# Kernel tuning notes

Hardware: AMD Instinct MI355X
Metric: run time of the kernel (lower is better)

Reference implementation:

```python
import jax, jax.numpy as jnp
import numpy as np

N = 100000
E = 1600000
CIN = 32
COUT = 32
K = 5
EPS = 1e-15      # PyG GMMConv EPS in sigma^2 denominator
BN_EPS = 1e-5    # torch BatchNorm1d default eps


def gmm_conv(x, edge_index, edge_attr, g, mu, sigma, root, bias):
    """PyG GMMConv (MoNet), aggr='mean', root_weight=True, bias=True."""
    src, dst = edge_index[0], edge_index[1]
    n = x.shape[0]
    k = mu.shape[0]
    cout = root.shape[1]
    xg = (x @ g).reshape(n, k, cout)                # [N, K, out]
    xj = xg[src]                                    # gather: [E, K, out]
    d = edge_attr[:, None, :] - mu[None, :, :]      # [E, K, 3]
    w = jnp.exp(-0.5 * jnp.sum(d * d / (EPS + sigma[None] ** 2), axis=-1))  # [E, K]
    msg = jnp.einsum('eko,ek->eo', xj, w)           # [E, out]
    agg = jax.ops.segment_sum(msg, dst, num_segments=n)
    cnt = jax.ops.segment_sum(jnp.ones((msg.shape[0],), x.dtype), dst, num_segments=n)
    agg = agg / jnp.clip(cnt, 1.0)[:, None]         # mean aggregation
    return agg + x @ root + bias


def batch_norm(x, gamma, beta):
    # training-mode BatchNorm1d: biased batch statistics over node dim
    m = x.mean(0)
    v = x.var(0)
    return (x - m) * jax.lax.rsqrt(v + BN_EPS) * gamma + beta


def setup_inputs() -> dict:
    key = jax.random.key(0)
    ks = jax.random.split(key, 12)
    p = lambda k, s, sc=0.1: jax.random.normal(k, s, jnp.float32) * sc
    return {
        'x': jax.random.normal(ks[0], (N, CIN), jnp.float32),
        'edge_index': jax.random.randint(ks[1], (2, E), 0, N, jnp.int32),
        'edge_attr': jax.random.uniform(ks[2], (E, 3), jnp.float32),
        # left conv1: in -> out, K=5
        'g1': p(ks[3], (CIN, K * COUT)), 'mu1': p(ks[4], (K, 3), 1.0), 'sigma1': jnp.ones((K, 3), jnp.float32),
        'root1': p(ks[5], (CIN, COUT)), 'b1': jnp.zeros((COUT,), jnp.float32),
        'gam1': jnp.ones((COUT,), jnp.float32), 'bet1': jnp.zeros((COUT,), jnp.float32),
        # left conv2: out -> out, K=5
        'g2': p(ks[6], (COUT, K * COUT)), 'mu2': p(ks[7], (K, 3), 1.0), 'sigma2': jnp.ones((K, 3), jnp.float32),
        'root2': p(ks[8], (COUT, COUT)), 'b2': jnp.zeros((COUT,), jnp.float32),
        'gam2': jnp.ones((COUT,), jnp.float32), 'bet2': jnp.zeros((COUT,), jnp.float32),
        # shortcut conv: in -> out, K=1
        'gs': p(ks[9], (CIN, 1 * COUT)), 'mus': p(ks[10], (1, 3), 1.0), 'sigmas': jnp.ones((1, 3), jnp.float32),
        'roots': p(ks[11], (CIN, COUT)), 'bs': jnp.zeros((COUT,), jnp.float32),
        'gams': jnp.ones((COUT,), jnp.float32), 'bets': jnp.zeros((COUT,), jnp.float32),
    }


def reference(x, edge_index, edge_attr,
              g1, mu1, sigma1, root1, b1, gam1, bet1,
              g2, mu2, sigma2, root2, b2, gam2, bet2,
              gs, mus, sigmas, roots, bs, gams, bets):
    h = jax.nn.elu(batch_norm(gmm_conv(x, edge_index, edge_attr, g1, mu1, sigma1, root1, b1), gam1, bet1))
    h = batch_norm(gmm_conv(h, edge_index, edge_attr, g2, mu2, sigma2, root2, b2), gam2, bet2)
    s = batch_norm(gmm_conv(x, edge_index, edge_attr, gs, mus, sigmas, roots, bs), gams, bets)
    return jax.nn.elu(h + s)
```

## Files before the change

kernel.cpp:

```cpp
#include <hip/hip_runtime.h>
#include <hip/hip_bf16.h>
#include <math.h>


#define ELU(v) ((v) > 0.f ? (v) : (__expf(v) - 1.f))

using short8  = __attribute__((ext_vector_type(8))) short;
using floatx4 = __attribute__((ext_vector_type(4))) float;

__device__ inline ushort f2bf(float f) {
    __hip_bfloat16 h = __float2bfloat16(f);
    return *reinterpret_cast<ushort*>(&h);
}
__device__ inline float bflo(unsigned u) { return __uint_as_float(u << 16); }
__device__ inline float bfhi(unsigned u) { return __uint_as_float(u & 0xffff0000u); }
__device__ inline unsigned pack_bf2(float lo, float hi) {
    return ((unsigned)f2bf(hi) << 16) | (unsigned)f2bf(lo);
}

__global__ __launch_bounds__(256) void prep_a(
    const float* __restrict__ x, unsigned* __restrict__ AGGb, int N)
{
    const int idx = blockIdx.x * blockDim.x + threadIdx.x;
    if (idx >= N * 16) return;
    const int n = idx >> 4, l = idx & 15;
    const float2 p = ((const float2*)x)[idx];
    AGGb[(size_t)n * 112 + 96 + l] = pack_bf2(p.x, p.y);
}

__global__ __launch_bounds__(256) void prep_b(
    const float* __restrict__ out1, const float* __restrict__ coef,
    unsigned* __restrict__ AGGb, int N)
{
    const int idx = blockIdx.x * blockDim.x + threadIdx.x;
    if (idx >= N * 16) return;
    const int n = idx >> 4, l = idx & 15;
    const float2 p = ((const float2*)out1)[idx];
    const int c0 = 2 * l, c1 = 2 * l + 1;
    float v0 = p.x * coef[c0] + coef[32 + c0];
    float v1 = p.y * coef[c1] + coef[32 + c1];
    v0 = ELU(v0); v1 = ELU(v1);
    AGGb[(size_t)n * 96 + 80 + l] = pack_bf2(v0, v1);
}

#define CH 4096
__global__ __launch_bounds__(256) void binfill_k(
    const int* __restrict__ ei, const float* __restrict__ attr,
    int* __restrict__ gcur, unsigned long long* __restrict__ pay0,
    int E, int NB, int CAPc)
{
    __shared__ unsigned long long srec[CH];
    __shared__ unsigned char sbin[CH];
    __shared__ int cnt[256], offs[256], wcur[256], gbase[256], sc[256];

    const int t = threadIdx.x;
    const int e0 = blockIdx.x * CH;
    const int nrec = min(CH, E - e0);

    cnt[t] = 0;
    __syncthreads();

    unsigned long long rec[16];
    int bin[16];
#pragma unroll
    for (int r = 0; r < 16; ++r) {
        const int e = e0 + r * 256 + t;
        bin[r] = -1;
        if (e < E) {
            const int s = ei[e], d = ei[E + e];
            const float a0 = attr[(size_t)e * 3 + 0];
            const float a1 = attr[(size_t)e * 3 + 1];
            const float a2 = attr[(size_t)e * 3 + 2];
            const unsigned q0 = (unsigned)min(max((int)(a0 * 4096.f), 0), 4095);
            const unsigned q1 = (unsigned)min(max((int)(a1 * 4096.f), 0), 4095);
            const unsigned q2 = (unsigned)min(max((int)(a2 * 4096.f), 0), 4095);
            rec[r] = (unsigned long long)(unsigned)s
                   | ((unsigned long long)(d & 511) << 17)
                   | ((unsigned long long)q0 << 26)
                   | ((unsigned long long)q1 << 38)
                   | ((unsigned long long)q2 << 50);
            bin[r] = d >> 9;
            atomicAdd(&cnt[bin[r]], 1);
        }
    }
    __syncthreads();

    const int v = cnt[t];
    sc[t] = v;
    __syncthreads();
    for (int o = 1; o < 256; o <<= 1) {
        const int xx = (t >= o) ? sc[t - o] : 0;
        __syncthreads();
        sc[t] += xx;
        __syncthreads();
    }
    offs[t] = sc[t] - v;
    wcur[t] = sc[t] - v;
    __syncthreads();

#pragma unroll
    for (int r = 0; r < 16; ++r) {
        if (bin[r] >= 0) {
            const int pos = atomicAdd(&wcur[bin[r]], 1);
            srec[pos] = rec[r];
            sbin[pos] = (unsigned char)bin[r];
        }
    }
    __syncthreads();

    if (t < NB && cnt[t] > 0) gbase[t] = atomicAdd(&gcur[t], cnt[t]);
    __syncthreads();

    for (int i = t; i < nrec; i += 256) {
        const int b = sbin[i];
        const int idx = gbase[b] + (i - offs[b]);
        if (idx < CAPc)
            pay0[(size_t)b * CAPc + idx] = srec[i];
    }
}

__global__ void bucket_scan(const int* __restrict__ gcur, int* __restrict__ bbase,
                            int NB)
{
    __shared__ int sh[256];
    const int t = threadIdx.x;
    const int v = (t < NB) ? gcur[t] : 0;
    sh[t] = v;
    __syncthreads();
    for (int o = 1; o < 256; o <<= 1) {
        const int xx = (t >= o) ? sh[t - o] : 0;
        __syncthreads();
        sh[t] += xx;
        __syncthreads();
    }
    if (t < NB) bbase[t] = sh[t] - v;
}

__global__ __launch_bounds__(256) void scatter2_k(
    const unsigned long long* __restrict__ pay0, const int* __restrict__ gcur,
    const int* __restrict__ bbase, int* __restrict__ row_ptr,
    unsigned long long* __restrict__ pay, int N, int CAPc, int NB)
{
    const int b = blockIdx.x;
    const int t = threadIdx.x;
    const int d0 = b << 9;
    const int nd = min(512, N - d0);

    __shared__ int cnt[512];
    __shared__ int offs[512];
    __shared__ int sscan[256];

    for (int i = t; i < 512; i += 256) cnt[i] = 0;
    __syncthreads();

    const int total = min(gcur[b], CAPc);
    const unsigned long long* src = pay0 + (size_t)b * CAPc;

    for (int i = t; i < total; i += 256) {
        const int dlo = (int)((src[i] >> 17) & 511);
        atomicAdd(&cnt[dlo], 1);
    }
    __syncthreads();

    const int c0 = cnt[2 * t], c1 = cnt[2 * t + 1];
    const int pairsum = c0 + c1;
    sscan[t] = pairsum;
    __syncthreads();
    for (int o = 1; o < 256; o <<= 1) {
        const int xx = (t >= o) ? sscan[t - o] : 0;
        __syncthreads();
        sscan[t] += xx;
        __syncthreads();
    }
    const int excl = sscan[t] - pairsum;
    offs[2 * t] = excl;
    offs[2 * t + 1] = excl + c0;
    __syncthreads();
    const int btotal = sscan[255];

    const int base = bbase[b];
    for (int i = t; i < nd; i += 256) row_ptr[d0 + i] = base + offs[i];
    if (b == NB - 1 && t == 0) row_ptr[N] = base + btotal;

    for (int i = t; i < 512; i += 256) cnt[i] = offs[i];
    __syncthreads();

    for (int i = t; i < total; i += 256) {
        const unsigned long long rec = src[i];
        const int dlo = (int)((rec >> 17) & 511);
        const int p = atomicAdd(&cnt[dlo], 1);
        pay[base + p] = rec;
    }
}

template <int SLS, bool HAS_S>
__global__ __launch_bounds__(256) void gather_k(
    const unsigned* __restrict__ XB,
    const unsigned long long* __restrict__ payload,
    const int* __restrict__ row_ptr,
    const float* __restrict__ mu_m, const float* __restrict__ sg_m,
    const float* __restrict__ mu_s, const float* __restrict__ sg_s,
    unsigned* __restrict__ AGGb,
    int N, int ntiles)
{
    constexpr int KS = HAS_S ? 6 : 5;
    constexpr float DQ = 1.0f / 4096.0f;

    float mm[15], im[15];
#pragma unroll
    for (int i = 0; i < 15; ++i) {
        mm[i] = mu_m[i];
        float s = sg_m[i];
        im[i] = 1.0f / (1e-15f + s * s);
    }
    float ms[3], is[3];
    if (HAS_S) {
#pragma unroll
        for (int i = 0; i < 3; ++i) {
            ms[i] = mu_s[i];
            float s = sg_s[i];
            is[i] = 1.0f / (1e-15f + s * s);
        }
    }

    const int l = threadIdx.x & 15;
    const int g = threadIdx.x >> 4;
    __shared__ float wbuf[16][17][8];

    for (int tile = blockIdx.x; tile < ntiles; tile += gridDim.x) {
        const int dst = tile * 16 + g;
        float2 acc[KS];
#pragma unroll
        for (int k = 0; k < KS; ++k) acc[k] = make_float2(0.f, 0.f);

        int rp0 = 0, deg = 0;
        if (dst < N) { rp0 = row_ptr[dst]; deg = row_ptr[dst + 1] - rp0; }

        auto body = [&](int j) {
            const float4 a = *(const float4*)&wbuf[g][j][0];
            const float4 b = *(const float4*)&wbuf[g][j][4];
            const int sj = __float_as_int(a.x);
            const unsigned u = XB[(size_t)sj * 16 + l];
            const float x0 = bflo(u), x1 = bfhi(u);
            acc[0].x = fmaf(a.y, x0, acc[0].x); acc[0].y = fmaf(a.y, x1, acc[0].y);
            acc[1].x = fmaf(a.z, x0, acc[1].x); acc[1].y = fmaf(a.z, x1, acc[1].y);
            acc[2].x = fmaf(a.w, x0, acc[2].x); acc[2].y = fmaf(a.w, x1, acc[2].y);
            acc[3].x = fmaf(b.x, x0, acc[3].x); acc[3].y = fmaf(b.x, x1, acc[3].y);
            acc[4].x = fmaf(b.y, x0, acc[4].x); acc[4].y = fmaf(b.y, x1, acc[4].y);
            if (HAS_S) {
                acc[5].x = fmaf(b.z, x0, acc[5].x); acc[5].y = fmaf(b.z, x1, acc[5].y);
            }
        };

        for (int base = 0; base < deg; base += 16) {
            const int nj = min(16, deg - base);
            if (l < nj) {
                unsigned long long pq = payload[rp0 + base + l];
                const int src = (int)(pq & 0x1FFFFull);
                float p0 = ((int)((pq >> 26) & 0xFFF) + 0.5f) * DQ;
                float p1 = ((int)((pq >> 38) & 0xFFF) + 0.5f) * DQ;
                float p2 = ((int)((pq >> 50) & 0xFFF) + 0.5f) * DQ;
                float w[5], wS = 0.f;
#pragma unroll
                for (int k = 0; k < 5; ++k) {
                    float d0 = p0 - mm[k * 3 + 0];
                    float d1 = p1 - mm[k * 3 + 1];
                    float d2 = p2 - mm[k * 3 + 2];
                    float q = d0 * d0 * im[k * 3 + 0] + d1 * d1 * im[k * 3 + 1]
                            + d2 * d2 * im[k * 3 + 2];
                    w[k] = __expf(-0.5f * q);
                }
                if (HAS_S) {
                    float d0 = p0 - ms[0], d1 = p1 - ms[1], d2 = p2 - ms[2];
                    float q = d0 * d0 * is[0] + d1 * d1 * is[1] + d2 * d2 * is[2];
                    wS = __expf(-0.5f * q);
                }
                float4* wp = (float4*)&wbuf[g][l][0];
                wp[0] = make_float4(__int_as_float(src), w[0], w[1], w[2]);
                wp[1] = make_float4(w[3], w[4], wS, 0.f);
            }
            int j = 0;
            for (; j + 3 < nj; j += 4) { body(j); body(j + 1); body(j + 2); body(j + 3); }
            for (; j < nj; ++j) body(j);
        }

        if (dst < N) {
            const float invd = 1.0f / fmaxf((float)deg, 1.0f);
            unsigned* out = AGGb + (size_t)dst * (SLS * 16) + l;
#pragma unroll
            for (int k = 0; k < KS; ++k)
                out[k * 16] = pack_bf2(acc[k].x * invd, acc[k].y * invd);
        }
    }
}

template <bool HAS_S>
__global__ __launch_bounds__(256) void transform_k(
    const unsigned* __restrict__ AGGb,
    const float* __restrict__ g,
    const float* __restrict__ rootm,
    const float* __restrict__ bm,
    const float* __restrict__ gss,
    const float* __restrict__ rootss,
    const float* __restrict__ bss,
    float* __restrict__ out_m, float* __restrict__ out_s,
    float* __restrict__ stats_m, float* __restrict__ stats_s,
    int N)
{
    constexpr int SLS = HAS_S ? 7 : 6;
    const int lane = threadIdx.x & 63;
    const int l4 = lane & 15, quad = lane >> 4;
    const int wv = threadIdx.x >> 6;

    short8 Bc[6][2];
#pragma unroll
    for (int s = 0; s < 5; ++s)
#pragma unroll
        for (int t = 0; t < 2; ++t)
#pragma unroll
            for (int j = 0; j < 8; ++j)
                Bc[s][t][j] = (short)f2bf(g[(quad * 8 + j) * 160 + s * 32 + 16 * t + l4]);
#pragma unroll
    for (int t = 0; t < 2; ++t)
#pragma unroll
        for (int j = 0; j < 8; ++j)
            Bc[5][t][j] = (short)f2bf(rootm[(quad * 8 + j) * 32 + 16 * t + l4]);

    short8 Bs2[2][2];
    if (HAS_S) {
#pragma unroll
        for (int t = 0; t < 2; ++t)
#pragma unroll
            for (int j = 0; j < 8; ++j) {
                Bs2[0][t][j] = (short)f2bf(gss[(quad * 8 + j) * 32 + 16 * t + l4]);
                Bs2[1][t][j] = (short)f2bf(rootss[(quad * 8 + j) * 32 + 16 * t + l4]);
            }
    }

    const float bm0 = bm[l4], bm1 = bm[16 + l4];
    const float bs0 = HAS_S ? bss[l4] : 0.f;
    const float bs1 = HAS_S ? bss[16 + l4] : 0.f;

    const int ngroups = (N + 15) >> 4;
    float ps0 = 0, pq0 = 0, ps1 = 0, pq1 = 0;
    float psS0 = 0, pqS0 = 0, psS1 = 0, pqS1 = 0;

    for (int grp = blockIdx.x * 4 + wv; grp < ngroups; grp += gridDim.x * 4) {
        const int node0 = grp * 16;
        const int myn = min(node0 + l4, N - 1);
        const unsigned* arow = AGGb + (size_t)myn * (SLS * 16) + quad * 4;

        floatx4 acc0 = {0.f, 0.f, 0.f, 0.f}, acc1 = {0.f, 0.f, 0.f, 0.f};
#pragma unroll
        for (int s = 0; s < 6; ++s) {
            const int slot = (s < 5) ? s : (SLS - 1);
            const uint4 av = *(const uint4*)(arow + 16 * slot);
            const short8 A = *reinterpret_cast<const short8*>(&av);
            acc0 = __builtin_amdgcn_mfma_f32_16x16x32_bf16(A, Bc[s][0], acc0, 0, 0, 0);
            acc1 = __builtin_amdgcn_mfma_f32_16x16x32_bf16(A, Bc[s][1], acc1, 0, 0, 0);
        }
        floatx4 accS0 = {0.f, 0.f, 0.f, 0.f}, accS1 = {0.f, 0.f, 0.f, 0.f};
        if (HAS_S) {
#pragma unroll
            for (int s = 0; s < 2; ++s) {
                const int slot = 5 + s;
                const uint4 av = *(const uint4*)(arow + 16 * slot);
                const short8 A = *reinterpret_cast<const short8*>(&av);
                accS0 = __builtin_amdgcn_mfma_f32_16x16x32_bf16(A, Bs2[s][0], accS0, 0, 0, 0);
                accS1 = __builtin_amdgcn_mfma_f32_16x16x32_bf16(A, Bs2[s][1], accS1, 0, 0, 0);
            }
        }

#pragma unroll
        for (int r = 0; r < 4; ++r) {
            const int n = node0 + quad * 4 + r;
            if (n < N) {
                float v0 = acc0[r] + bm0;
                float v1 = acc1[r] + bm1;
                out_m[(size_t)n * 32 + l4] = v0;
                out_m[(size_t)n * 32 + 16 + l4] = v1;
                ps0 += v0; pq0 += v0 * v0;
                ps1 += v1; pq1 += v1 * v1;
                if (HAS_S) {
                    float s0 = accS0[r] + bs0;
                    float s1 = accS1[r] + bs1;
                    out_s[(size_t)n * 32 + l4] = s0;
                    out_s[(size_t)n * 32 + 16 + l4] = s1;
                    psS0 += s0; pqS0 += s0 * s0;
                    psS1 += s1; pqS1 += s1 * s1;
                }
            }
        }
    }

    __shared__ float sred[64];
    const int tid = threadIdx.x;
    const int spread = (blockIdx.x & 7) * 64;
    {
        if (tid < 64) sred[tid] = 0.f;
        __syncthreads();
        atomicAdd(&sred[l4], ps0);       atomicAdd(&sred[16 + l4], ps1);
        atomicAdd(&sred[32 + l4], pq0);  atomicAdd(&sred[48 + l4], pq1);
        __syncthreads();
        if (tid < 64) atomicAdd(&stats_m[spread + tid], sred[tid]);
        __syncthreads();
    }
    if (HAS_S) {
        if (tid < 64) sred[tid] = 0.f;
        __syncthreads();
        atomicAdd(&sred[l4], psS0);      atomicAdd(&sred[16 + l4], psS1);
        atomicAdd(&sred[32 + l4], pqS0); atomicAdd(&sred[48 + l4], pqS1);
        __syncthreads();
        if (tid < 64) atomicAdd(&stats_s[spread + tid], sred[tid]);
    }
}

__global__ void coef_k(const float* __restrict__ stats, const float* __restrict__ gam,
                       const float* __restrict__ bet, float* __restrict__ coef,
                       float invN)
{
    int c = threadIdx.x;
    if (c < 32) {
        float s = 0.f, q = 0.f;
        for (int p = 0; p < 8; ++p) { s += stats[p * 64 + c]; q += stats[p * 64 + 32 + c]; }
        float m = s * invN;
        float v = fmaxf(q * invN - m * m, 0.f);
        float sc = gam[c] * rsqrtf(v + 1e-5f);
        coef[c] = sc;
        coef[32 + c] = bet[c] - m * sc;
    }
}

__global__ __launch_bounds__(256) void final_k(
    const float* __restrict__ o2, const float* __restrict__ os,
    const float* __restrict__ c2, const float* __restrict__ cs,
    float* __restrict__ out, int total)
{
    int idx = blockIdx.x * blockDim.x + threadIdx.x;
    if (idx >= total) return;
    int c = idx & 31;
    float v = o2[idx] * c2[c] + c2[32 + c] + os[idx] * cs[c] + cs[32 + c];
    out[idx] = ELU(v);
}

extern "C" void kernel_launch(void* const* d_in, const int* in_sizes, int n_in,
                              void* d_out, int out_size, void* d_ws, size_t ws_size,
                              hipStream_t stream)
{
    const float* x      = (const float*)d_in[0];
    const int*   ei     = (const int*)d_in[1];
    const float* attr   = (const float*)d_in[2];
    const float* g1     = (const float*)d_in[3];
    const float* mu1    = (const float*)d_in[4];
    const float* sig1   = (const float*)d_in[5];
    const float* root1  = (const float*)d_in[6];
    const float* b1     = (const float*)d_in[7];
    const float* gam1   = (const float*)d_in[8];
    const float* bet1   = (const float*)d_in[9];
    const float* g2     = (const float*)d_in[10];
    const float* mu2    = (const float*)d_in[11];
    const float* sig2   = (const float*)d_in[12];
    const float* root2  = (const float*)d_in[13];
    const float* b2     = (const float*)d_in[14];
    const float* gam2   = (const float*)d_in[15];
    const float* bet2   = (const float*)d_in[16];
    const float* gs     = (const float*)d_in[17];
    const float* mus    = (const float*)d_in[18];
    const float* sigs   = (const float*)d_in[19];
    const float* roots  = (const float*)d_in[20];
    const float* bs     = (const float*)d_in[21];
    const float* gams   = (const float*)d_in[22];
    const float* bets   = (const float*)d_in[23];

    const int N = in_sizes[0] / 32;
    const int E = in_sizes[1] / 2;
    const int total = N * 32;
    const int ntiles = (N + 15) / 16;
    const int NB = (N + 511) >> 9;
    const int CAPc = ((((E + NB - 1) / NB) * 5) / 4 + 15) & ~15;

    char* ws = (char*)d_ws;
    size_t off = 0;
    auto carve = [&](size_t bytes) {
        void* p = ws + off;
        off = (off + bytes + 255) & ~(size_t)255;
        return p;
    };
    unsigned* XB   = (unsigned*)carve((size_t)N * 16 * 4);
    unsigned* AGGb = (unsigned*)carve((size_t)N * 112 * 4);
    float*  OUT1   = (float*)carve((size_t)N * 32 * 4);
    float*  OUT2   = (float*)carve((size_t)N * 32 * 4);
    float*  OUTS   = (float*)carve((size_t)N * 32 * 4);
    unsigned long long* PAY  = (unsigned long long*)carve((size_t)E * 8);
    unsigned long long* PAY0 = (unsigned long long*)carve((size_t)NB * CAPc * 8);
    int*    ROWP   = (int*)carve((size_t)(N + 1) * 4);
    int*    GCUR   = (int*)carve(512 * 4);
    int*    BBASE  = GCUR + 256;
    float*  STATS  = (float*)carve(3 * 512 * 4);
    float*  COEF   = (float*)carve(3 * 64 * 4);
    float* stats1 = STATS, *stats2 = STATS + 512, *statsS = STATS + 1024;
    float* coef1 = COEF, *coef2 = COEF + 64, *coefS = COEF + 128;
    (void)ws_size; (void)n_in; (void)out_size;

    const float invN = 1.0f / (float)N;
    const int ew = (total + 255) / 256;
    const int epb = (N * 16 + 255) / 256;
    const int nfb = (E + CH - 1) / CH;

    hipMemsetAsync(GCUR, 0, 256 * 4, stream);
    hipMemsetAsync(STATS, 0, 3 * 512 * 4, stream);

    binfill_k<<<nfb, 256, 0, stream>>>(ei, attr, GCUR, PAY0, E, NB, CAPc);
    bucket_scan<<<1, 256, 0, stream>>>(GCUR, BBASE, NB);
    scatter2_k<<<NB, 256, 0, stream>>>(PAY0, GCUR, BBASE, ROWP, PAY, N, CAPc, NB);

    prep_a<<<epb, 256, 0, stream>>>(x, AGGb, N);
    {
    }
    extern __global__ void prep_xb(const float*, unsigned*, int);
    prep_xb<<<epb, 256, 0, stream>>>(x, XB, N);

    gather_k<7, true><<<ntiles, 256, 0, stream>>>(XB, PAY, ROWP,
        mu1, sig1, mus, sigs, AGGb, N, ntiles);
    transform_k<true><<<1024, 256, 0, stream>>>(AGGb, g1, root1, b1,
        gs, roots, bs, OUT1, OUTS, stats1, statsS, N);
    coef_k<<<1, 64, 0, stream>>>(stats1, gam1, bet1, coef1, invN);
    coef_k<<<1, 64, 0, stream>>>(statsS, gams, bets, coefS, invN);

    prep_b<<<epb, 256, 0, stream>>>(OUT1, coef1, AGGb, N);
    extern __global__ void prep_hxb(const float*, const float*, unsigned*, int);
    prep_hxb<<<epb, 256, 0, stream>>>(OUT1, coef1, XB, N);
    gather_k<6, false><<<ntiles, 256, 0, stream>>>(XB, PAY, ROWP,
        mu2, sig2, nullptr, nullptr, AGGb, N, ntiles);
    transform_k<false><<<1024, 256, 0, stream>>>(AGGb, g2, root2, b2,
        nullptr, nullptr, nullptr, OUT2, nullptr, stats2, nullptr, N);
    coef_k<<<1, 64, 0, stream>>>(stats2, gam2, bet2, coef2, invN);

    final_k<<<ew, 256, 0, stream>>>(OUT2, OUTS, coef2, coefS, (float*)d_out, total);
}

__global__ __launch_bounds__(256) void prep_xb(
    const float* __restrict__ x, unsigned* __restrict__ XB, int N)
{
    const int idx = blockIdx.x * blockDim.x + threadIdx.x;
    if (idx >= N * 16) return;
    const float2 p = ((const float2*)x)[idx];
    XB[idx] = pack_bf2(p.x, p.y);
}

__global__ __launch_bounds__(256) void prep_hxb(
    const float* __restrict__ out1, const float* __restrict__ coef,
    unsigned* __restrict__ XB, int N)
{
    const int idx = blockIdx.x * blockDim.x + threadIdx.x;
    if (idx >= N * 16) return;
    const int l = idx & 15;
    const float2 p = ((const float2*)out1)[idx];
    const int c0 = 2 * l, c1 = 2 * l + 1;
    float v0 = p.x * coef[c0] + coef[32 + c0];
    float v1 = p.y * coef[c1] + coef[32 + c1];
    v0 = ELU(v0); v1 = ELU(v1);
    XB[idx] = pack_bf2(v0, v1);
}
```

Before: 326.5 us.

## Fuse edge gather and MFMA transform into one kernel via shared-memory staging

Merges the per-destination gather/aggregation kernel and the MFMA feature-transform kernel into a single kernel. Each block aggregates 16 nodes into a shared-memory tile and then applies the bf16 MFMA transform directly from LDS. This removes the AGGb global round-trip and the prep_a/prep_b copy kernels. The cost is extra LDS use, a block barrier between the two phases, and one tile per block instead of a persistent loop, so some waves sit idle during the MMA phase.

```diff
diff --git a/kernel.cpp b/kernel.cpp
--- a/kernel.cpp
+++ b/kernel.cpp
@@ -18,29 +18,28 @@
     return ((unsigned)f2bf(hi) << 16) | (unsigned)f2bf(lo);
 }
 
-__global__ __launch_bounds__(256) void prep_a(
-    const float* __restrict__ x, unsigned* __restrict__ AGGb, int N)
+__global__ __launch_bounds__(256) void prep_xb(
+    const float* __restrict__ x, unsigned* __restrict__ XB, int N)
 {
     const int idx = blockIdx.x * blockDim.x + threadIdx.x;
     if (idx >= N * 16) return;
-    const int n = idx >> 4, l = idx & 15;
     const float2 p = ((const float2*)x)[idx];
-    AGGb[(size_t)n * 112 + 96 + l] = pack_bf2(p.x, p.y);
-}
-
-__global__ __launch_bounds__(256) void prep_b(
+    XB[idx] = pack_bf2(p.x, p.y);
+}
+
+__global__ __launch_bounds__(256) void prep_hxb(
     const float* __restrict__ out1, const float* __restrict__ coef,
-    unsigned* __restrict__ AGGb, int N)
+    unsigned* __restrict__ XB, int N)
 {
     const int idx = blockIdx.x * blockDim.x + threadIdx.x;
     if (idx >= N * 16) return;
-    const int n = idx >> 4, l = idx & 15;
+    const int l = idx & 15;
     const float2 p = ((const float2*)out1)[idx];
     const int c0 = 2 * l, c1 = 2 * l + 1;
     float v0 = p.x * coef[c0] + coef[32 + c0];
     float v1 = p.y * coef[c1] + coef[32 + c1];
     v0 = ELU(v0); v1 = ELU(v1);
-    AGGb[(size_t)n * 96 + 80 + l] = pack_bf2(v0, v1);
+    XB[idx] = pack_bf2(v0, v1);
 }
 
 #define CH 4096
@@ -193,110 +192,13 @@
     }
 }
 
-template <int SLS, bool HAS_S>
-__global__ __launch_bounds__(256) void gather_k(
+template <bool HAS_S>
+__global__ __launch_bounds__(256) void gt_k(
     const unsigned* __restrict__ XB,
     const unsigned long long* __restrict__ payload,
     const int* __restrict__ row_ptr,
     const float* __restrict__ mu_m, const float* __restrict__ sg_m,
     const float* __restrict__ mu_s, const float* __restrict__ sg_s,
-    unsigned* __restrict__ AGGb,
-    int N, int ntiles)
-{
-    constexpr int KS = HAS_S ? 6 : 5;
-    constexpr float DQ = 1.0f / 4096.0f;
-
-    float mm[15], im[15];
-#pragma unroll
-    for (int i = 0; i < 15; ++i) {
-        mm[i] = mu_m[i];
-        float s = sg_m[i];
-        im[i] = 1.0f / (1e-15f + s * s);
-    }
-    float ms[3], is[3];
-    if (HAS_S) {
-#pragma unroll
-        for (int i = 0; i < 3; ++i) {
-            ms[i] = mu_s[i];
-            float s = sg_s[i];
-            is[i] = 1.0f / (1e-15f + s * s);
-        }
-    }
-
-    const int l = threadIdx.x & 15;
-    const int g = threadIdx.x >> 4;
-    __shared__ float wbuf[16][17][8];
-
-    for (int tile = blockIdx.x; tile < ntiles; tile += gridDim.x) {
-        const int dst = tile * 16 + g;
-        float2 acc[KS];
-#pragma unroll
-        for (int k = 0; k < KS; ++k) acc[k] = make_float2(0.f, 0.f);
-
-        int rp0 = 0, deg = 0;
-        if (dst < N) { rp0 = row_ptr[dst]; deg = row_ptr[dst + 1] - rp0; }
-
-        auto body = [&](int j) {
-            const float4 a = *(const float4*)&wbuf[g][j][0];
-            const float4 b = *(const float4*)&wbuf[g][j][4];
-            const int sj = __float_as_int(a.x);
-            const unsigned u = XB[(size_t)sj * 16 + l];
-            const float x0 = bflo(u), x1 = bfhi(u);
-            acc[0].x = fmaf(a.y, x0, acc[0].x); acc[0].y = fmaf(a.y, x1, acc[0].y);
-            acc[1].x = fmaf(a.z, x0, acc[1].x); acc[1].y = fmaf(a.z, x1, acc[1].y);
-            acc[2].x = fmaf(a.w, x0, acc[2].x); acc[2].y = fmaf(a.w, x1, acc[2].y);
-            acc[3].x = fmaf(b.x, x0, acc[3].x); acc[3].y = fmaf(b.x, x1, acc[3].y);
-            acc[4].x = fmaf(b.y, x0, acc[4].x); acc[4].y = fmaf(b.y, x1, acc[4].y);
-            if (HAS_S) {
-                acc[5].x = fmaf(b.z, x0, acc[5].x); acc[5].y = fmaf(b.z, x1, acc[5].y);
-            }
-        };
-
-        for (int base = 0; base < deg; base += 16) {
-            const int nj = min(16, deg - base);
-            if (l < nj) {
-                unsigned long long pq = payload[rp0 + base + l];
-                const int src = (int)(pq & 0x1FFFFull);
-                float p0 = ((int)((pq >> 26) & 0xFFF) + 0.5f) * DQ;
-                float p1 = ((int)((pq >> 38) & 0xFFF) + 0.5f) * DQ;
-                float p2 = ((int)((pq >> 50) & 0xFFF) + 0.5f) * DQ;
-                float w[5], wS = 0.f;
-#pragma unroll
-                for (int k = 0; k < 5; ++k) {
-                    float d0 = p0 - mm[k * 3 + 0];
-                    float d1 = p1 - mm[k * 3 + 1];
-                    float d2 = p2 - mm[k * 3 + 2];
-                    float q = d0 * d0 * im[k * 3 + 0] + d1 * d1 * im[k * 3 + 1]
-                            + d2 * d2 * im[k * 3 + 2];
-                    w[k] = __expf(-0.5f * q);
-                }
-                if (HAS_S) {
-                    float d0 = p0 - ms[0], d1 = p1 - ms[1], d2 = p2 - ms[2];
-                    float q = d0 * d0 * is[0] + d1 * d1 * is[1] + d2 * d2 * is[2];
-                    wS = __expf(-0.5f * q);
-                }
-                float4* wp = (float4*)&wbuf[g][l][0];
-                wp[0] = make_float4(__int_as_float(src), w[0], w[1], w[2]);
-                wp[1] = make_float4(w[3], w[4], wS, 0.f);
-            }
-            int j = 0;
-            for (; j + 3 < nj; j += 4) { body(j); body(j + 1); body(j + 2); body(j + 3); }
-            for (; j < nj; ++j) body(j);
-        }
-
-        if (dst < N) {
-            const float invd = 1.0f / fmaxf((float)deg, 1.0f);
-            unsigned* out = AGGb + (size_t)dst * (SLS * 16) + l;
-#pragma unroll
-            for (int k = 0; k < KS; ++k)
-                out[k * 16] = pack_bf2(acc[k].x * invd, acc[k].y * invd);
-        }
-    }
-}
-
-template <bool HAS_S>
-__global__ __launch_bounds__(256) void transform_k(
-    const unsigned* __restrict__ AGGb,
     const float* __restrict__ g,
     const float* __restrict__ rootm,
     const float* __restrict__ bm,
@@ -307,112 +209,170 @@
     float* __restrict__ stats_m, float* __restrict__ stats_s,
     int N)
 {
-    constexpr int SLS = HAS_S ? 7 : 6;
-    const int lane = threadIdx.x & 63;
-    const int l4 = lane & 15, quad = lane >> 4;
-    const int wv = threadIdx.x >> 6;
-
-    short8 Bc[6][2];
-#pragma unroll
-    for (int s = 0; s < 5; ++s)
-#pragma unroll
-        for (int t = 0; t < 2; ++t)
+    constexpr int KS = HAS_S ? 6 : 5;
+    constexpr int SLS = KS + 1;
+    constexpr int STRIDE = SLS * 16 + 4;
+    constexpr float DQ = 1.0f / 4096.0f;
+
+    __shared__ float wbuf[16][17][8];
+    __shared__ unsigned sA[16 * STRIDE];
+    __shared__ float sred[128];
+
+    const int tid = threadIdx.x;
+    const int l = tid & 15, grp = tid >> 4;
+    const int lane = tid & 63, l4 = lane & 15, quad = lane >> 4;
+    const int wv = tid >> 6;
+    const int half = wv & 1;
+
+    if (tid < 128) sred[tid] = 0.f;
+
+    const bool convRole = (wv < 2);
+    const bool sRole = HAS_S && (wv >= 2);
+    short8 Bf[6];
+    float bias0 = 0.f;
+    if (convRole) {
+#pragma unroll
+        for (int s = 0; s < 5; ++s)
 #pragma unroll
             for (int j = 0; j < 8; ++j)
-                Bc[s][t][j] = (short)f2bf(g[(quad * 8 + j) * 160 + s * 32 + 16 * t + l4]);
-#pragma unroll
-    for (int t = 0; t < 2; ++t)
+                Bf[s][j] = (short)f2bf(g[(quad * 8 + j) * 160 + s * 32 + 16 * half + l4]);
 #pragma unroll
         for (int j = 0; j < 8; ++j)
-            Bc[5][t][j] = (short)f2bf(rootm[(quad * 8 + j) * 32 + 16 * t + l4]);
-
-    short8 Bs2[2][2];
+            Bf[5][j] = (short)f2bf(rootm[(quad * 8 + j) * 32 + 16 * half + l4]);
+        bias0 = bm[16 * half + l4];
+    } else if (sRole) {
+#pragma unroll
+        for (int j = 0; j < 8; ++j) {
+            Bf[0][j] = (short)f2bf(gss[(quad * 8 + j) * 32 + 16 * half + l4]);
+            Bf[1][j] = (short)f2bf(rootss[(quad * 8 + j) * 32 + 16 * half + l4]);
+        }
+        bias0 = bss[16 * half + l4];
+    }
+
+    float mm[15], im[15];
+#pragma unroll
+    for (int i = 0; i < 15; ++i) {
+        mm[i] = mu_m[i];
+        float s = sg_m[i];
+        im[i] = 1.0f / (1e-15f + s * s);
+    }
+    float ms[3], is[3];
     if (HAS_S) {
 #pragma unroll
-        for (int t = 0; t < 2; ++t)
-#pragma unroll
-            for (int j = 0; j < 8; ++j) {
-                Bs2[0][t][j] = (short)f2bf(gss[(quad * 8 + j) * 32 + 16 * t + l4]);
-                Bs2[1][t][j] = (short)f2bf(rootss[(quad * 8 + j) * 32 + 16 * t + l4]);
+        for (int i = 0; i < 3; ++i) {
+            ms[i] = mu_s[i];
+            float s = sg_s[i];
+            is[i] = 1.0f / (1e-15f + s * s);
+        }
+    }
+
+    const int dst = blockIdx.x * 16 + grp;
+    float2 acc[KS];
+#pragma unroll
+    for (int k = 0; k < KS; ++k) acc[k] = make_float2(0.f, 0.f);
+
+    int rp0 = 0, deg = 0;
+    if (dst < N) { rp0 = row_ptr[dst]; deg = row_ptr[dst + 1] - rp0; }
+
+    auto body = [&](int j) {
+        const float4 a = *(const float4*)&wbuf[grp][j][0];
+        const float4 b = *(const float4*)&wbuf[grp][j][4];
+        const int sj = __float_as_int(a.x);
+        const unsigned u = XB[(size_t)sj * 16 + l];
+        const float x0 = bflo(u), x1 = bfhi(u);
+        acc[0].x = fmaf(a.y, x0, acc[0].x); acc[0].y = fmaf(a.y, x1, acc[0].y);
+        acc[1].x = fmaf(a.z, x0, acc[1].x); acc[1].y = fmaf(a.z, x1, acc[1].y);
+        acc[2].x = fmaf(a.w, x0, acc[2].x); acc[2].y = fmaf(a.w, x1, acc[2].y);
+        acc[3].x = fmaf(b.x, x0, acc[3].x); acc[3].y = fmaf(b.x, x1, acc[3].y);
+        acc[4].x = fmaf(b.y, x0, acc[4].x); acc[4].y = fmaf(b.y, x1, acc[4].y);
+        if (HAS_S) {
+            acc[5].x = fmaf(b.z, x0, acc[5].x); acc[5].y = fmaf(b.z, x1, acc[5].y);
+        }
+    };
+
+    for (int base = 0; base < deg; base += 16) {
+        const int nj = min(16, deg - base);
+        if (l < nj) {
+            unsigned long long pq = payload[rp0 + base + l];
+            const int src = (int)(pq & 0x1FFFFull);
+            float p0 = ((int)((pq >> 26) & 0xFFF) + 0.5f) * DQ;
+            float p1 = ((int)((pq >> 38) & 0xFFF) + 0.5f) * DQ;
+            float p2 = ((int)((pq >> 50) & 0xFFF) + 0.5f) * DQ;
+            float w[5], wS = 0.f;
+#pragma unroll
+            for (int k = 0; k < 5; ++k) {
+                float d0 = p0 - mm[k * 3 + 0];
+                float d1 = p1 - mm[k * 3 + 1];
+                float d2 = p2 - mm[k * 3 + 2];
+                float q = d0 * d0 * im[k * 3 + 0] + d1 * d1 * im[k * 3 + 1]
+                        + d2 * d2 * im[k * 3 + 2];
+                w[k] = __expf(-0.5f * q);
             }
-    }
-
-    const float bm0 = bm[l4], bm1 = bm[16 + l4];
-    const float bs0 = HAS_S ? bss[l4] : 0.f;
-    const float bs1 = HAS_S ? bss[16 + l4] : 0.f;
-
-    const int ngroups = (N + 15) >> 4;
-    float ps0 = 0, pq0 = 0, ps1 = 0, pq1 = 0;
-    float psS0 = 0, pqS0 = 0, psS1 = 0, pqS1 = 0;
-
-    for (int grp = blockIdx.x * 4 + wv; grp < ngroups; grp += gridDim.x * 4) {
-        const int node0 = grp * 16;
-        const int myn = min(node0 + l4, N - 1);
-        const unsigned* arow = AGGb + (size_t)myn * (SLS * 16) + quad * 4;
-
-        floatx4 acc0 = {0.f, 0.f, 0.f, 0.f}, acc1 = {0.f, 0.f, 0.f, 0.f};
-#pragma unroll
-        for (int s = 0; s < 6; ++s) {
-            const int slot = (s < 5) ? s : (SLS - 1);
-            const uint4 av = *(const uint4*)(arow + 16 * slot);
-            const short8 A = *reinterpret_cast<const short8*>(&av);
-            acc0 = __builtin_amdgcn_mfma_f32_16x16x32_bf16(A, Bc[s][0], acc0, 0, 0, 0);
-            acc1 = __builtin_amdgcn_mfma_f32_16x16x32_bf16(A, Bc[s][1], acc1, 0, 0, 0);
-        }
-        floatx4 accS0 = {0.f, 0.f, 0.f, 0.f}, accS1 = {0.f, 0.f, 0.f, 0.f};
-        if (HAS_S) {
+            if (HAS_S) {
+                float d0 = p0 - ms[0], d1 = p1 - ms[1], d2 = p2 - ms[2];
+                float q = d0 * d0 * is[0] + d1 * d1 * is[1] + d2 * d2 * is[2];
+                wS = __expf(-0.5f * q);
+            }
+            float4* wp = (float4*)&wbuf[grp][l][0];
+            wp[0] = make_float4(__int_as_float(src), w[0], w[1], w[2]);
+            wp[1] = make_float4(w[3], w[4], wS, 0.f);
+        }
+        int j = 0;
+        for (; j + 3 < nj; j += 4) { body(j); body(j + 1); body(j + 2); body(j + 3); }
+        for (; j < nj; ++j) body(j);
+    }
+
+    {
+        unsigned* arow = sA + grp * STRIDE;
+        const float invd = 1.0f / fmaxf((float)deg, 1.0f);
+        const bool ok = (dst < N);
+#pragma unroll
+        for (int k = 0; k < KS; ++k)
+            arow[k * 16 + l] = ok ? pack_bf2(acc[k].x * invd, acc[k].y * invd) : 0u;
+        arow[KS * 16 + l] = ok ? XB[(size_t)dst * 16 + l] : 0u;
+    }
+    __syncthreads();
+
+    if (convRole || sRole) {
+        floatx4 C = {0.f, 0.f, 0.f, 0.f};
+        if (convRole) {
+#pragma unroll
+            for (int s = 0; s < 6; ++s) {
+                const int slot = (s < 5) ? s : KS;
+                const uint4 av = *(const uint4*)(sA + l4 * STRIDE + slot * 16 + quad * 4);
+                const short8 A = *reinterpret_cast<const short8*>(&av);
+                C = __builtin_amdgcn_mfma_f32_16x16x32_bf16(A, Bf[s], C, 0, 0, 0);
+            }
+        } else {
 #pragma unroll
             for (int s = 0; s < 2; ++s) {
                 const int slot = 5 + s;
-                const uint4 av = *(const uint4*)(arow + 16 * slot);
+                const uint4 av = *(const uint4*)(sA + l4 * STRIDE + slot * 16 + quad * 4);
                 const short8 A = *reinterpret_cast<const short8*>(&av);
-                accS0 = __builtin_amdgcn_mfma_f32_16x16x32_bf16(A, Bs2[s][0], accS0, 0, 0, 0);
-                accS1 = __builtin_amdgcn_mfma_f32_16x16x32_bf16(A, Bs2[s][1], accS1, 0, 0, 0);
+                C = __builtin_amdgcn_mfma_f32_16x16x32_bf16(A, Bf[s], C, 0, 0, 0);
             }
         }
 
+        float* outp = convRole ? out_m : out_s;
+        float ps = 0.f, pq = 0.f;
 #pragma unroll
         for (int r = 0; r < 4; ++r) {
-            const int n = node0 + quad * 4 + r;
+            const int n = blockIdx.x * 16 + quad * 4 + r;
             if (n < N) {
-                float v0 = acc0[r] + bm0;
-                float v1 = acc1[r] + bm1;
-                out_m[(size_t)n * 32 + l4] = v0;
-                out_m[(size_t)n * 32 + 16 + l4] = v1;
-                ps0 += v0; pq0 += v0 * v0;
-                ps1 += v1; pq1 += v1 * v1;
-                if (HAS_S) {
-                    float s0 = accS0[r] + bs0;
-                    float s1 = accS1[r] + bs1;
-                    out_s[(size_t)n * 32 + l4] = s0;
-                    out_s[(size_t)n * 32 + 16 + l4] = s1;
-                    psS0 += s0; pqS0 += s0 * s0;
-                    psS1 += s1; pqS1 += s1 * s1;
-                }
+                const float v = C[r] + bias0;
+                outp[(size_t)n * 32 + 16 * half + l4] = v;
+                ps += v; pq += v * v;
             }
         }
-    }
-
-    __shared__ float sred[64];
-    const int tid = threadIdx.x;
+        const int base = convRole ? 0 : 64;
+        atomicAdd(&sred[base + 16 * half + l4], ps);
+        atomicAdd(&sred[base + 32 + 16 * half + l4], pq);
+    }
+    __syncthreads();
+
     const int spread = (blockIdx.x & 7) * 64;
-    {
-        if (tid < 64) sred[tid] = 0.f;
-        __syncthreads();
-        atomicAdd(&sred[l4], ps0);       atomicAdd(&sred[16 + l4], ps1);
-        atomicAdd(&sred[32 + l4], pq0);  atomicAdd(&sred[48 + l4], pq1);
-        __syncthreads();
-        if (tid < 64) atomicAdd(&stats_m[spread + tid], sred[tid]);
-        __syncthreads();
-    }
-    if (HAS_S) {
-        if (tid < 64) sred[tid] = 0.f;
-        __syncthreads();
-        atomicAdd(&sred[l4], psS0);      atomicAdd(&sred[16 + l4], psS1);
-        atomicAdd(&sred[32 + l4], pqS0); atomicAdd(&sred[48 + l4], pqS1);
-        __syncthreads();
-        if (tid < 64) atomicAdd(&stats_s[spread + tid], sred[tid]);
-    }
+    if (tid < 64) atomicAdd(&stats_m[spread + tid], sred[tid]);
+    else if (HAS_S && tid < 128) atomicAdd(&stats_s[spread + tid - 64], sred[tid]);
 }
 
 __global__ void coef_k(const float* __restrict__ stats, const float* __restrict__ gam,
@@ -487,7 +447,6 @@
         return p;
     };
     unsigned* XB   = (unsigned*)carve((size_t)N * 16 * 4);
-    unsigned* AGGb = (unsigned*)carve((size_t)N * 112 * 4);
     float*  OUT1   = (float*)carve((size_t)N * 32 * 4);
     float*  OUT2   = (float*)carve((size_t)N * 32 * 4);
     float*  OUTS   = (float*)carve((size_t)N * 32 * 4);
@@ -514,51 +473,18 @@
     bucket_scan<<<1, 256, 0, stream>>>(GCUR, BBASE, NB);
     scatter2_k<<<NB, 256, 0, stream>>>(PAY0, GCUR, BBASE, ROWP, PAY, N, CAPc, NB);
 
-    prep_a<<<epb, 256, 0, stream>>>(x, AGGb, N);
-    {
-    }
-    extern __global__ void prep_xb(const float*, unsigned*, int);
     prep_xb<<<epb, 256, 0, stream>>>(x, XB, N);
-
-    gather_k<7, true><<<ntiles, 256, 0, stream>>>(XB, PAY, ROWP,
-        mu1, sig1, mus, sigs, AGGb, N, ntiles);
-    transform_k<true><<<1024, 256, 0, stream>>>(AGGb, g1, root1, b1,
-        gs, roots, bs, OUT1, OUTS, stats1, statsS, N);
+    gt_k<true><<<ntiles, 256, 0, stream>>>(XB, PAY, ROWP,
+        mu1, sig1, mus, sigs, g1, root1, b1, gs, roots, bs,
+        OUT1, OUTS, stats1, statsS, N);
     coef_k<<<1, 64, 0, stream>>>(stats1, gam1, bet1, coef1, invN);
     coef_k<<<1, 64, 0, stream>>>(statsS, gams, bets, coefS, invN);
 
-    prep_b<<<epb, 256, 0, stream>>>(OUT1, coef1, AGGb, N);
-    extern __global__ void prep_hxb(const float*, const float*, unsigned*, int);
     prep_hxb<<<epb, 256, 0, stream>>>(OUT1, coef1, XB, N);
-    gather_k<6, false><<<ntiles, 256, 0, stream>>>(XB, PAY, ROWP,
-        mu2, sig2, nullptr, nullptr, AGGb, N, ntiles);
-    transform_k<false><<<1024, 256, 0, stream>>>(AGGb, g2, root2, b2,
-        nullptr, nullptr, nullptr, OUT2, nullptr, stats2, nullptr, N);
+    gt_k<false><<<ntiles, 256, 0, stream>>>(XB, PAY, ROWP,
+        mu2, sig2, nullptr, nullptr, g2, root2, b2, nullptr, nullptr, nullptr,
+        OUT2, nullptr, stats2, nullptr, N);
     coef_k<<<1, 64, 0, stream>>>(stats2, gam2, bet2, coef2, invN);
 
     final_k<<<ew, 256, 0, stream>>>(OUT2, OUTS, coef2, coefS, (float*)d_out, total);
 }
-
-__global__ __launch_bounds__(256) void prep_xb(
-    const float* __restrict__ x, unsigned* __restrict__ XB, int N)
-{
-    const int idx = blockIdx.x * blockDim.x + threadIdx.x;
-    if (idx >= N * 16) return;
-    const float2 p = ((const float2*)x)[idx];
-    XB[idx] = pack_bf2(p.x, p.y);
-}
-
-__global__ __launch_bounds__(256) void prep_hxb(
-    const float* __restrict__ out1, const float* __restrict__ coef,
-    unsigned* __restrict__ XB, int N)
-{
-    const int idx = blockIdx.x * blockDim.x + threadIdx.x;
-    if (idx >= N * 16) return;
-    const int l = idx & 15;
-    const float2 p = ((const float2*)out1)[idx];
-    const int c0 = 2 * l, c1 = 2 * l + 1;
-    float v0 = p.x * coef[c0] + coef[32 + c0];
-    float v1 = p.y * coef[c1] + coef[32 + c1];
-    v0 = ELU(v0); v1 = ELU(v1);
-    XB[idx] = pack_bf2(v0, v1);
-}
```

After: 326.4 us. Within noise of the previous version (-0.0%).
